# Kernel optimization log

Hardware: AMD Instinct MI355X
Metric: run time of the kernel (lower is better)

Reference implementation:

```python
import jax, jax.numpy as jnp
import numpy as np

N_NODES = 50000
N_EDGES = 800000
NUM_GRAPHS = 64
NEG_SLOPE = 0.2


def gatv2_layer(x, src, dst, Wl, bl, Wr, br, att, b_out, heads, out_ch, concat):
    # PyG GATv2Conv: x_j = lin_l(x)[src], x_i = lin_r(x)[dst]
    N = x.shape[0]
    xl = (x @ Wl + bl).reshape(N, heads, out_ch)
    xr = (x @ Wr + br).reshape(N, heads, out_ch)
    m = xl[src] + xr[dst]                                  # [E, H, C]
    e = jax.nn.leaky_relu(m, negative_slope=NEG_SLOPE)
    logits = jnp.einsum('ehc,hc->eh', e, att)              # [E, H]
    # softmax over incoming edges of each destination node
    seg_max = jax.ops.segment_max(logits, dst, num_segments=N)
    ex = jnp.exp(logits - seg_max[dst])
    denom = jax.ops.segment_sum(ex, dst, num_segments=N)
    alpha = ex / denom[dst]                                # [E, H]
    out = jax.ops.segment_sum(alpha[..., None] * xl[src], dst, num_segments=N)
    out = out.reshape(N, heads * out_ch) if concat else out.mean(axis=1)
    return out + b_out


def _forward(x, edge_index, batch,
             Wl1, bl1, Wr1, br1, att1, b1,
             Wl2, bl2, Wr2, br2, att2, b2,
             Wl3, bl3, Wr3, br3, att3, b3,
             Wm1, bm1, Wm2, bm2):
    N = x.shape[0]
    loops = jnp.arange(N, dtype=edge_index.dtype)
    src = jnp.concatenate([edge_index[0], loops])          # add_self_loops=True
    dst = jnp.concatenate([edge_index[1], loops])
    h = jax.nn.relu(gatv2_layer(x, src, dst, Wl1, bl1, Wr1, br1, att1, b1, 4, 64, True))
    h = jax.nn.relu(gatv2_layer(h, src, dst, Wl2, bl2, Wr2, br2, att2, b2, 2, 64, True))
    h = jax.nn.relu(gatv2_layer(h, src, dst, Wl3, bl3, Wr3, br3, att3, b3, 1, 64, False))
    # global_mean_pool
    sums = jax.ops.segment_sum(h, batch, num_segments=NUM_GRAPHS)
    counts = jax.ops.segment_sum(jnp.ones((N, 1), h.dtype), batch, num_segments=NUM_GRAPHS)
    pooled = sums / jnp.maximum(counts, 1.0)
    return jax.nn.relu(pooled @ Wm1 + bm1) @ Wm2 + bm2


def setup_inputs() -> dict:
    key = jax.random.key(0)
    ks = jax.random.split(key, 24)
    s = 0.05
    inp = {
        'x': jax.random.normal(ks[0], (N_NODES, 128), jnp.float32),
        'edge_index': jax.random.randint(ks[1], (2, N_EDGES), 0, N_NODES, jnp.int64),
        'batch': jnp.sort(jax.random.randint(ks[2], (N_NODES,), 0, NUM_GRAPHS, jnp.int64)),
        # conv1: in=128, heads=4, C=64
        'Wl1': jax.random.normal(ks[3], (128, 256), jnp.float32) * s,
        'bl1': jnp.zeros((256,), jnp.float32),
        'Wr1': jax.random.normal(ks[4], (128, 256), jnp.float32) * s,
        'br1': jnp.zeros((256,), jnp.float32),
        'att1': jax.random.normal(ks[5], (4, 64), jnp.float32) * s,
        'b1': jnp.zeros((256,), jnp.float32),
        # conv2: in=256, heads=2, C=64
        'Wl2': jax.random.normal(ks[6], (256, 128), jnp.float32) * s,
        'bl2': jnp.zeros((128,), jnp.float32),
        'Wr2': jax.random.normal(ks[7], (256, 128), jnp.float32) * s,
        'br2': jnp.zeros((128,), jnp.float32),
        'att2': jax.random.normal(ks[8], (2, 64), jnp.float32) * s,
        'b2': jnp.zeros((128,), jnp.float32),
        # conv3: in=128, heads=1, C=64, concat=False
        'Wl3': jax.random.normal(ks[9], (128, 64), jnp.float32) * s,
        'bl3': jnp.zeros((64,), jnp.float32),
        'Wr3': jax.random.normal(ks[10], (128, 64), jnp.float32) * s,
        'br3': jnp.zeros((64,), jnp.float32),
        'att3': jax.random.normal(ks[11], (1, 64), jnp.float32) * s,
        'b3': jnp.zeros((64,), jnp.float32),
        # MLP 64 -> 32 -> 2
        'Wm1': jax.random.normal(ks[12], (64, 32), jnp.float32) * s,
        'bm1': jnp.zeros((32,), jnp.float32),
        'Wm2': jax.random.normal(ks[13], (32, 2), jnp.float32) * s,
        'bm2': jnp.zeros((2,), jnp.float32),
    }
    return inp


def reference(x, edge_index, batch,
              Wl1, bl1, Wr1, br1, att1, b1,
              Wl2, bl2, Wr2, br2, att2, b2,
              Wl3, bl3, Wr3, br3, att3, b3,
              Wm1, bm1, Wm2, bm2):
    return _forward(x, edge_index, batch,
                    Wl1, bl1, Wr1, br1, att1, b1,
                    Wl2, bl2, Wr2, br2, att2, b2,
                    Wl3, bl3, Wr3, br3, att3, b3,
                    Wm1, bm1, Wm2, bm2)
```

## Files before the change

### kernel.cpp

```cpp
#include <hip/hip_runtime.h>


typedef __attribute__((ext_vector_type(8))) short bf16x8;
typedef __attribute__((ext_vector_type(4))) float f32x4;

#define SORT_BLOCKS 64
#define SCAN_BLOCKS 256

__device__ inline unsigned short f2bf(float f) {
    unsigned u = __float_as_uint(f);
    unsigned r = (u + 0x7fff + ((u >> 16) & 1)) >> 16;
    return (unsigned short)r;
}

__device__ inline void unpack8(uint4 a, float* d) {
    d[0] = __uint_as_float(a.x << 16); d[1] = __uint_as_float(a.x & 0xffff0000u);
    d[2] = __uint_as_float(a.y << 16); d[3] = __uint_as_float(a.y & 0xffff0000u);
    d[4] = __uint_as_float(a.z << 16); d[5] = __uint_as_float(a.z & 0xffff0000u);
    d[6] = __uint_as_float(a.w << 16); d[7] = __uint_as_float(a.w & 0xffff0000u);
}

__global__ void cvt_kernel(const float* __restrict__ in,
                           unsigned short* __restrict__ out, int n)
{
    int i = (blockIdx.x * blockDim.x + threadIdx.x) * 4;
    if (i >= n) return;
    float4 v = *reinterpret_cast<const float4*>(in + i);
    ushort4 o;
    o.x = f2bf(v.x); o.y = f2bf(v.y); o.z = f2bf(v.z); o.w = f2bf(v.w);
    *reinterpret_cast<ushort4*>(out + i) = o;
}

__global__ void cvt_wt_all_kernel(
    const float* __restrict__ Wl1, const float* __restrict__ Wr1, unsigned short* __restrict__ T1l, unsigned short* __restrict__ T1r,
    const float* __restrict__ Wl2, const float* __restrict__ Wr2, unsigned short* __restrict__ T2l, unsigned short* __restrict__ T2r,
    const float* __restrict__ Wl3, const float* __restrict__ Wr3, unsigned short* __restrict__ T3l, unsigned short* __restrict__ T3r)
{
    int id = blockIdx.x * blockDim.x + threadIdx.x;
    const float* W; unsigned short* T; int K, No, idx;
    if (id < 2 * 32768) {
        K = 128; No = 256; idx = id & 32767;
        W = (id < 32768) ? Wl1 : Wr1; T = (id < 32768) ? T1l : T1r;
    } else if (id < 2 * 32768 + 2 * 32768) {
        int v = id - 65536; K = 256; No = 128; idx = v & 32767;
        W = (v < 32768) ? Wl2 : Wr2; T = (v < 32768) ? T2l : T2r;
    } else {
        int v = id - 131072; if (v >= 2 * 8192) return;
        K = 128; No = 64; idx = v & 8191;
        W = (v < 8192) ? Wl3 : Wr3; T = (v < 8192) ? T3l : T3r;
    }
    int n = idx / K, k = idx - n * K;
    T[idx] = f2bf(W[(size_t)k * No + n]);
}

template <int K, int NY>
__global__ __launch_bounds__(256) void gemm_slab(
    const unsigned short* __restrict__ A,
    const unsigned short* __restrict__ W0, const unsigned short* __restrict__ W1,
    const float* __restrict__ bias0, const float* __restrict__ bias1,
    unsigned short* __restrict__ OutL, unsigned short* __restrict__ OutR,
    int M)
{
    constexpr int CPR = K / 8;
    __shared__ __align__(16) char As[64 * K * 2];
    __shared__ __align__(16) char Bs[64 * 128 * 2];

    const int t = threadIdx.x;
    const int lane = t & 63;
    const int wid = t >> 6;
    const int row0 = blockIdx.x * 64;

    #pragma unroll
    for (int i = 0; i < (64 * CPR) / 256; ++i) {
        int c16 = i * 256 + t;
        int r = c16 / CPR, j = c16 % CPR;
        int gr = row0 + r; if (gr > M - 1) gr = M - 1;
        uint4 v = *reinterpret_cast<const uint4*>(A + (size_t)gr * K + j * 8);
        *reinterpret_cast<uint4*>(As + r * (2 * K) + ((j ^ (r & 7)) << 4)) = v;
    }

    const int ra = wid * 16 + (lane & 15);
    const int rowA_byte = ra * (2 * K);

    for (int z = 0; z < 2; ++z) {
        const unsigned short* Wt = z ? W1 : W0;
        const float* bias = z ? bias1 : bias0;
        unsigned short* Out = z ? OutR : OutL;
        for (int y = 0; y < NY; ++y) {
            f32x4 acc[4];
            #pragma unroll
            for (int j = 0; j < 4; ++j) acc[j] = (f32x4){0.f, 0.f, 0.f, 0.f};

            #pragma unroll
            for (int kh = 0; kh < K / 128; ++kh) {
                __syncthreads();
                #pragma unroll
                for (int i = 0; i < 4; ++i) {
                    int c16 = i * 256 + t;
                    int n = c16 >> 4, j = c16 & 15;
                    uint4 v = *reinterpret_cast<const uint4*>(
                        Wt + (size_t)(y * 64 + n) * K + kh * 128 + j * 8);
                    *reinterpret_cast<uint4*>(Bs + n * 256 + ((j ^ (n & 7)) << 4)) = v;
                }
                __syncthreads();
                #pragma unroll
                for (int ks = 0; ks < 4; ++ks) {
                    int chA = kh * 16 + ks * 4 + (lane >> 4);
                    bf16x8 a = *reinterpret_cast<const bf16x8*>(
                        As + rowA_byte + ((chA ^ (ra & 7)) << 4));
                    #pragma unroll
                    for (int j = 0; j < 4; ++j) {
                        int nb = j * 16 + (lane & 15);
                        int chB = ks * 4 + (lane >> 4);
                        bf16x8 b = *reinterpret_cast<const bf16x8*>(
                            Bs + nb * 256 + ((chB ^ (nb & 7)) << 4));
                        acc[j] = __builtin_amdgcn_mfma_f32_16x16x32_bf16(a, b, acc[j], 0, 0, 0);
                    }
                }
            }
            __syncthreads();
            #pragma unroll
            for (int j = 0; j < 4; ++j) {
                float bb = bias[y * 64 + j * 16 + (lane & 15)];
                #pragma unroll
                for (int q = 0; q < 4; ++q) {
                    int r = wid * 16 + (lane >> 4) * 4 + q;
                    int c = j * 16 + (lane & 15);
                    *reinterpret_cast<unsigned short*>(Bs + r * 128 + c * 2)
                        = f2bf(acc[j][q] + bb);
                }
            }
            __syncthreads();
            {
                int r = t >> 2, ch = t & 3;
                int gr = row0 + r;
                if (gr < M) {
                    const uint4* src = reinterpret_cast<const uint4*>(Bs + r * 128 + ch * 32);
                    uint4 v0 = src[0], v1 = src[1];
                    uint4* dst = reinterpret_cast<uint4*>(
                        Out + ((size_t)y * M + gr) * 64 + ch * 16);
                    dst[0] = v0; dst[1] = v1;
                }
            }
        }
    }
}

__global__ void hist_kernel(const int* __restrict__ ei, int E, int Etot,
                            int* __restrict__ deg)
{
    int i = blockIdx.x * blockDim.x + threadIdx.x;
    if (i >= Etot) return;
    int d = (i < E) ? ei[E + i] : (i - E);
    atomicAdd(&deg[d], 1);
}

__global__ __launch_bounds__(256) void scan1_kernel(
    const int* __restrict__ deg, int* __restrict__ blockSums, int N)
{
    __shared__ int red[256];
    const int b = blockIdx.x, t = threadIdx.x;
    const int chunk = (N + SCAN_BLOCKS - 1) / SCAN_BLOCKS;
    const int lo = b * chunk;
    const int hi = (lo + chunk < N) ? lo + chunk : N;
    int s = 0;
    for (int i = lo + t; i < hi; i += 256) s += deg[i];
    red[t] = s;
    __syncthreads();
    #pragma unroll
    for (int off = 128; off > 0; off >>= 1) {
        if (t < off) red[t] += red[t + off];
        __syncthreads();
    }
    if (t == 0) blockSums[b] = red[0];
}

__global__ __launch_bounds__(256) void scan2_kernel(
    const int* __restrict__ blockSums, int* __restrict__ blockBase,
    int* __restrict__ rowptr, int N)
{
    __shared__ int tmp[256];
    const int t = threadIdx.x;
    int v = blockSums[t];
    tmp[t] = v;
    __syncthreads();
    for (int off = 1; off < 256; off <<= 1) {
        int u = (t >= off) ? tmp[t - off] : 0;
        __syncthreads();
        tmp[t] += u;
        __syncthreads();
    }
    blockBase[t] = tmp[t] - v;
    if (t == 255) rowptr[N] = tmp[255];
}

__global__ __launch_bounds__(256) void scan3_kernel(
    const int* __restrict__ deg, const int* __restrict__ blockBase,
    int* __restrict__ rowptr, int* __restrict__ cursor, int N)
{
    __shared__ int tmp[256];
    __shared__ int carry;
    const int b = blockIdx.x, t = threadIdx.x;
    const int chunk = (N + SCAN_BLOCKS - 1) / SCAN_BLOCKS;
    const int lo = b * chunk;
    const int hi = (lo + chunk < N) ? lo + chunk : N;
    if (t == 0) carry = blockBase[b];
    __syncthreads();
    for (int j = lo; j < hi; j += 256) {
        int i = j + t;
        int v = (i < hi) ? deg[i] : 0;
        tmp[t] = v;
        __syncthreads();
        for (int off = 1; off < 256; off <<= 1) {
            int u = (t >= off) ? tmp[t - off] : 0;
            __syncthreads();
            tmp[t] += u;
            __syncthreads();
        }
        int excl = carry + tmp[t] - v;
        if (i < hi) { rowptr[i] = excl; cursor[i] = excl; }
        __syncthreads();
        if (t == 255) carry += tmp[255];
        __syncthreads();
    }
}

__global__ void scatter_kernel(const int* __restrict__ ei, int E, int Etot,
                               int* __restrict__ cursor, int* __restrict__ ssrc)
{
    int i = blockIdx.x * blockDim.x + threadIdx.x;
    if (i >= Etot) return;
    int d, s;
    if (i < E) { s = ei[i]; d = ei[E + i]; }
    else       { s = i - E; d = s; }
    int pos = atomicAdd(&cursor[d], 1);
    ssrc[pos] = s;
}

__global__ __launch_bounds__(256) void dhist2_kernel(
    const int* __restrict__ rowptr, int* __restrict__ blockHist, int N)
{
    __shared__ int lh[256];
    lh[threadIdx.x] = 0;
    __syncthreads();
    const int chunk = (N + SORT_BLOCKS - 1) / SORT_BLOCKS;
    const int lo = blockIdx.x * chunk;
    const int hi = (lo + chunk < N) ? lo + chunk : N;
    for (int d = lo + threadIdx.x; d < hi; d += 256) {
        int deg = rowptr[d + 1] - rowptr[d];
        atomicAdd(&lh[deg > 255 ? 255 : deg], 1);
    }
    __syncthreads();
    blockHist[blockIdx.x * 256 + threadIdx.x] = lh[threadIdx.x];
}

__global__ __launch_bounds__(256) void dscan2_kernel(
    const int* __restrict__ blockHist, int* __restrict__ blockOff)
{
    const int t = threadIdx.x;
    int total = 0;
    for (int b = 0; b < SORT_BLOCKS; ++b) total += blockHist[b * 256 + t];
    __shared__ int tmp[256];
    tmp[t] = total;
    __syncthreads();
    for (int off = 1; off < 256; off <<= 1) {
        int v = (t >= off) ? tmp[t - off] : 0;
        __syncthreads();
        tmp[t] += v;
        __syncthreads();
    }
    int grand = tmp[255];
    int start = grand - tmp[t];
    for (int b = 0; b < SORT_BLOCKS; ++b) {
        blockOff[b * 256 + t] = start;
        start += blockHist[b * 256 + t];
    }
}

__global__ __launch_bounds__(256) void dscatter2_kernel(
    const int* __restrict__ rowptr, const int* __restrict__ blockOff,
    int* __restrict__ dperm, int N)
{
    __shared__ int cur[256];
    cur[threadIdx.x] = blockOff[blockIdx.x * 256 + threadIdx.x];
    __syncthreads();
    const int chunk = (N + SORT_BLOCKS - 1) / SORT_BLOCKS;
    const int lo = blockIdx.x * chunk;
    const int hi = (lo + chunk < N) ? lo + chunk : N;
    for (int d = lo + threadIdx.x; d < hi; d += 256) {
        int deg = rowptr[d + 1] - rowptr[d];
        int pos = atomicAdd(&cur[deg > 255 ? 255 : deg], 1);
        dperm[pos] = d;
    }
}

template <int H, bool OUT_F32, bool OUT_BF16>
__global__ __launch_bounds__(256) void gat_fused4(
    const int* __restrict__ rowptr, const int* __restrict__ ssrc,
    const int* __restrict__ dperm,
    const unsigned short* __restrict__ xl, const unsigned short* __restrict__ xr,
    const float* __restrict__ att, const float* __restrict__ bias,
    float* __restrict__ outf, unsigned short* __restrict__ outb, int N)
{
    const int gid = blockIdx.x * 64 + (threadIdx.x >> 2);
    const int sub = threadIdx.x & 3;
    if (gid >= N * H) return;
    const int h  = gid / N;
    const int di = gid - h * N;
    const int d  = dperm[di];
    const int HC = H * 64;
    const int so = sub * 16;

    const unsigned short* xlh = xl + (size_t)h * N * 64;

    float xrv[16], attv[16], acc[16];
    {
        const unsigned short* pr = xr + ((size_t)h * N + d) * 64 + so;
        uint4 v0 = *reinterpret_cast<const uint4*>(pr);
        uint4 v1 = *reinterpret_cast<const uint4*>(pr + 8);
        unpack8(v0, xrv); unpack8(v1, xrv + 8);
        const float* pa = att + h * 64 + so;
        #pragma unroll
        for (int k = 0; k < 16; k += 4) {
            float4 w = *reinterpret_cast<const float4*>(pa + k);
            attv[k] = w.x; attv[k+1] = w.y; attv[k+2] = w.z; attv[k+3] = w.w;
        }
    }
    #pragma unroll
    for (int k = 0; k < 16; ++k) acc[k] = 0.f;
    float M = -3.0e38f, S = 0.f;

    const int begin = rowptr[d], end = rowptr[d + 1];
    uint4 c0, c1;
    {
        const unsigned short* pl = xlh + (size_t)ssrc[begin] * 64 + so;
        c0 = *reinterpret_cast<const uint4*>(pl);
        c1 = *reinterpret_cast<const uint4*>(pl + 8);
    }
    for (int e = begin; e < end; ++e) {
        uint4 n0, n1;
        const bool more = (e + 1 < end);
        if (more) {
            const unsigned short* pl = xlh + (size_t)ssrc[e + 1] * 64 + so;
            n0 = *reinterpret_cast<const uint4*>(pl);
            n1 = *reinterpret_cast<const uint4*>(pl + 8);
        }
        float cur[16];
        unpack8(c0, cur);
        unpack8(c1, cur + 8);
        float p = 0.f;
        #pragma unroll
        for (int k = 0; k < 16; ++k) {
            float v = cur[k] + xrv[k];
            v = fmaxf(v, 0.2f * v);
            p = fmaf(v, attv[k], p);
        }
        p += __shfl_xor(p, 1);
        p += __shfl_xor(p, 2);
        float nM = fmaxf(M, p);
        float scale = __expf(M - nM);
        float w = __expf(p - nM);
        S = fmaf(S, scale, w);
        #pragma unroll
        for (int k = 0; k < 16; ++k) acc[k] = fmaf(acc[k], scale, w * cur[k]);
        M = nM;
        if (more) { c0 = n0; c1 = n1; }
    }
    float inv = 1.f / S;
    const float* pb = bias + h * 64 + so;
    #pragma unroll
    for (int k = 0; k < 16; ++k) {
        float val = fmaf(acc[k], inv, pb[k]);
        acc[k] = val > 0.f ? val : 0.f;
    }
    size_t ob = (size_t)d * HC + h * 64 + so;
    if (OUT_F32) {
        #pragma unroll
        for (int k = 0; k < 16; k += 4) {
            float4 v = {acc[k], acc[k+1], acc[k+2], acc[k+3]};
            *reinterpret_cast<float4*>(outf + ob + k) = v;
        }
    }
    if (OUT_BF16) {
        unsigned pk[8];
        #pragma unroll
        for (int k = 0; k < 8; ++k)
            pk[k] = (unsigned)f2bf(acc[2*k]) | ((unsigned)f2bf(acc[2*k+1]) << 16);
        uint4 lo = {pk[0], pk[1], pk[2], pk[3]};
        uint4 hi = {pk[4], pk[5], pk[6], pk[7]};
        *reinterpret_cast<uint4*>(outb + ob) = lo;
        *reinterpret_cast<uint4*>(outb + ob + 8) = hi;
    }
}

__global__ __launch_bounds__(256) void pool_kernel2(
    const float* __restrict__ h3, const int* __restrict__ batch,
    float* __restrict__ sums, float* __restrict__ counts, int N)
{
    const int wave = blockIdx.x * 4 + (threadIdx.x >> 6);
    const int lane = threadIdx.x & 63;
    const int n0 = wave * 64;
    if (n0 >= N) return;
    const int n1 = (n0 + 64 < N) ? n0 + 64 : N;
    float s = 0.f, cnt = 0.f;
    int g = batch[n0];
    for (int n = n0; n < n1; ++n) {
        int gn = batch[n];
        if (gn != g) {
            atomicAdd(&sums[g * 64 + lane], s);
            if (lane == 0) atomicAdd(&counts[g], cnt);
            s = 0.f; cnt = 0.f; g = gn;
        }
        s += h3[(size_t)n * 64 + lane];
        cnt += 1.f;
    }
    atomicAdd(&sums[g * 64 + lane], s);
    if (lane == 0) atomicAdd(&counts[g], cnt);
}

__global__ __launch_bounds__(64) void mlp_kernel(
    const float* __restrict__ sums, const float* __restrict__ counts,
    const float* __restrict__ Wm1, const float* __restrict__ bm1,
    const float* __restrict__ Wm2, const float* __restrict__ bm2,
    float* __restrict__ out)
{
    int g = blockIdx.x;
    int t = threadIdx.x;
    __shared__ float pooled[64];
    __shared__ float hidden[32];
    float cnt = counts[g];
    cnt = cnt > 1.f ? cnt : 1.f;
    pooled[t] = sums[g * 64 + t] / cnt;
    __syncthreads();
    if (t < 32) {
        float a = bm1[t];
        #pragma unroll
        for (int k = 0; k < 64; ++k) a = fmaf(pooled[k], Wm1[k * 32 + t], a);
        hidden[t] = a > 0.f ? a : 0.f;
    }
    __syncthreads();
    if (t < 2) {
        float a = bm2[t];
        #pragma unroll
        for (int j = 0; j < 32; ++j) a = fmaf(hidden[j], Wm2[j * 2 + t], a);
        out[g * 2 + t] = a;
    }
}

static void run_layer(const unsigned short* Xb, int K, int H,
                      const float* bl, const float* br,
                      const float* att, const float* bias_out,
                      const unsigned short* Wtl, const unsigned short* Wtr,
                      const int* rowptr, const int* ssrc, const int* dperm, int N,
                      unsigned short* xl, unsigned short* xr,
                      float* houtf, unsigned short* houtb,
                      hipStream_t stream)
{
    int gblocks = (N + 63) / 64;
    if (K == 128 && H == 4)
        gemm_slab<128, 4><<<gblocks, 256, 0, stream>>>(Xb, Wtl, Wtr, bl, br, xl, xr, N);
    else if (K == 256)
        gemm_slab<256, 2><<<gblocks, 256, 0, stream>>>(Xb, Wtl, Wtr, bl, br, xl, xr, N);
    else
        gemm_slab<128, 1><<<gblocks, 256, 0, stream>>>(Xb, Wtl, Wtr, bl, br, xl, xr, N);

    int ngroups = N * H;
    int blocks = (ngroups + 63) / 64;
    if (H == 4)
        gat_fused4<4, false, true><<<blocks, 256, 0, stream>>>(
            rowptr, ssrc, dperm, xl, xr, att, bias_out, houtf, houtb, N);
    else if (H == 2)
        gat_fused4<2, false, true><<<blocks, 256, 0, stream>>>(
            rowptr, ssrc, dperm, xl, xr, att, bias_out, houtf, houtb, N);
    else
        gat_fused4<1, true, false><<<blocks, 256, 0, stream>>>(
            rowptr, ssrc, dperm, xl, xr, att, bias_out, houtf, houtb, N);
}

extern "C" void kernel_launch(void* const* d_in, const int* in_sizes, int n_in,
                              void* d_out, int out_size, void* d_ws, size_t ws_size,
                              hipStream_t stream)
{
    const float* x    = (const float*)d_in[0];
    const int*   ei   = (const int*)d_in[1];
    const int*   batch= (const int*)d_in[2];
    const float* Wl1 = (const float*)d_in[3];
    const float* bl1 = (const float*)d_in[4];
    const float* Wr1 = (const float*)d_in[5];
    const float* br1 = (const float*)d_in[6];
    const float* att1= (const float*)d_in[7];
    const float* b1  = (const float*)d_in[8];
    const float* Wl2 = (const float*)d_in[9];
    const float* bl2 = (const float*)d_in[10];
    const float* Wr2 = (const float*)d_in[11];
    const float* br2 = (const float*)d_in[12];
    const float* att2= (const float*)d_in[13];
    const float* b2  = (const float*)d_in[14];
    const float* Wl3 = (const float*)d_in[15];
    const float* bl3 = (const float*)d_in[16];
    const float* Wr3 = (const float*)d_in[17];
    const float* br3 = (const float*)d_in[18];
    const float* att3= (const float*)d_in[19];
    const float* b3  = (const float*)d_in[20];
    const float* Wm1 = (const float*)d_in[21];
    const float* bm1 = (const float*)d_in[22];
    const float* Wm2 = (const float*)d_in[23];
    const float* bm2 = (const float*)d_in[24];

    const int N    = in_sizes[2];
    const int E    = in_sizes[1] / 2;
    const int Etot = E + N;
    const int K1   = in_sizes[0] / N;

    char* wsb = (char*)d_ws;
    size_t o = 0;
    auto alloc = [&](size_t bytes) { char* p = wsb + o; o += (bytes + 255) & ~(size_t)255; return p; };
    unsigned short* xl    = (unsigned short*)alloc((size_t)N * 256 * 2);
    unsigned short* xr    = (unsigned short*)alloc((size_t)N * 256 * 2);
    unsigned short* xb    = (unsigned short*)alloc((size_t)N * K1 * 2);
    unsigned short* h1b   = (unsigned short*)alloc((size_t)N * 256 * 2);
    unsigned short* h2b   = (unsigned short*)alloc((size_t)N * 128 * 2);
    float*          h3f   = (float*)alloc((size_t)N * 64 * 4);
    int*   deg    = (int*)alloc((size_t)N * 4);
    int*   rowptr = (int*)alloc((size_t)(N + 1) * 4);
    int*   cursor = (int*)alloc((size_t)N * 4);
    int*   ssrc   = (int*)alloc((size_t)Etot * 4);
    int*   dperm  = (int*)alloc((size_t)N * 4);
    int*   blockHist = (int*)alloc((size_t)SORT_BLOCKS * 256 * 4);
    int*   blockOff  = (int*)alloc((size_t)SORT_BLOCKS * 256 * 4);
    int*   blockSums = (int*)alloc((size_t)SCAN_BLOCKS * 4);
    int*   blockBase = (int*)alloc((size_t)SCAN_BLOCKS * 4);
    unsigned short* Wt1l = (unsigned short*)alloc(128 * 256 * 2);
    unsigned short* Wt1r = (unsigned short*)alloc(128 * 256 * 2);
    unsigned short* Wt2l = (unsigned short*)alloc(256 * 128 * 2);
    unsigned short* Wt2r = (unsigned short*)alloc(256 * 128 * 2);
    unsigned short* Wt3l = (unsigned short*)alloc(128 * 64 * 2);
    unsigned short* Wt3r = (unsigned short*)alloc(128 * 64 * 2);
    float* sums   = (float*)alloc(64 * 64 * 4);
    float* counts = (float*)alloc(64 * 4);
    (void)ws_size; (void)n_in; (void)out_size;

    hipMemsetAsync(deg, 0, (size_t)N * 4, stream);
    hist_kernel<<<(Etot + 255) / 256, 256, 0, stream>>>(ei, E, Etot, deg);
    scan1_kernel<<<SCAN_BLOCKS, 256, 0, stream>>>(deg, blockSums, N);
    scan2_kernel<<<1, 256, 0, stream>>>(blockSums, blockBase, rowptr, N);
    scan3_kernel<<<SCAN_BLOCKS, 256, 0, stream>>>(deg, blockBase, rowptr, cursor, N);
    scatter_kernel<<<(Etot + 255) / 256, 256, 0, stream>>>(ei, E, Etot, cursor, ssrc);
    dhist2_kernel<<<SORT_BLOCKS, 256, 0, stream>>>(rowptr, blockHist, N);
    dscan2_kernel<<<1, 256, 0, stream>>>(blockHist, blockOff);
    dscatter2_kernel<<<SORT_BLOCKS, 256, 0, stream>>>(rowptr, blockOff, dperm, N);

    cvt_kernel<<<((N * K1) / 4 + 255) / 256, 256, 0, stream>>>(x, xb, N * K1);
    cvt_wt_all_kernel<<<(147456 + 255) / 256, 256, 0, stream>>>(
        Wl1, Wr1, Wt1l, Wt1r, Wl2, Wr2, Wt2l, Wt2r, Wl3, Wr3, Wt3l, Wt3r);

    run_layer(xb, K1, 4, bl1, br1, att1, b1, Wt1l, Wt1r,
              rowptr, ssrc, dperm, N, xl, xr, nullptr, h1b, stream);
    run_layer(h1b, 256, 2, bl2, br2, att2, b2, Wt2l, Wt2r,
              rowptr, ssrc, dperm, N, xl, xr, nullptr, h2b, stream);
    run_layer(h2b, 128, 1, bl3, br3, att3, b3, Wt3l, Wt3r,
              rowptr, ssrc, dperm, N, xl, xr, h3f, nullptr, stream);

    hipMemsetAsync(sums, 0, 64 * 64 * 4, stream);
    hipMemsetAsync(counts, 0, 64 * 4, stream);
    {
        int waves = (N + 63) / 64;
        pool_kernel2<<<(waves + 3) / 4, 256, 0, stream>>>(h3f, batch, sums, counts, N);
    }
    mlp_kernel<<<64, 64, 0, stream>>>(sums, counts, Wm1, bm1, Wm2, bm2, (float*)d_out);
}
```

Before: 357.2 us.

## Switch intermediates from bf16 to fp16 and use packed half math in edge loop

Changes all intermediate activations and weights from bf16 to fp16, uses the fp16 MFMA in the projection GEMM, and rewrites the per-edge attention loop to use packed half2 add/max/mul and fdot2 instead of unpacking to fp32. The aim is to halve the ALU work per edge in the gather-bound attention kernel while keeping the same memory traffic. The risk is lower range: the softmax accumulator is kept in fp16, which can lose precision or overflow with large activations.

```diff
diff --git a/kernel.cpp b/kernel.cpp
--- a/kernel.cpp
+++ b/kernel.cpp
@@ -1,43 +1,37 @@
 #include <hip/hip_runtime.h>
 
 
-typedef __attribute__((ext_vector_type(8))) short bf16x8;
-typedef __attribute__((ext_vector_type(4))) float f32x4;
+typedef _Float16 half_t;
+typedef _Float16 h2    __attribute__((ext_vector_type(2)));
+typedef _Float16 f16x8 __attribute__((ext_vector_type(8)));
+typedef float    f32x4 __attribute__((ext_vector_type(4)));
 
 #define SORT_BLOCKS 64
 #define SCAN_BLOCKS 256
 
-__device__ inline unsigned short f2bf(float f) {
-    unsigned u = __float_as_uint(f);
-    unsigned r = (u + 0x7fff + ((u >> 16) & 1)) >> 16;
-    return (unsigned short)r;
-}
-
-__device__ inline void unpack8(uint4 a, float* d) {
-    d[0] = __uint_as_float(a.x << 16); d[1] = __uint_as_float(a.x & 0xffff0000u);
-    d[2] = __uint_as_float(a.y << 16); d[3] = __uint_as_float(a.y & 0xffff0000u);
-    d[4] = __uint_as_float(a.z << 16); d[5] = __uint_as_float(a.z & 0xffff0000u);
-    d[6] = __uint_as_float(a.w << 16); d[7] = __uint_as_float(a.w & 0xffff0000u);
-}
+#if __has_builtin(__builtin_amdgcn_fdot2)
+#define FDOT2(a, b, c) __builtin_amdgcn_fdot2((a), (b), (c), false)
+#else
+#define FDOT2(a, b, c) ((c) + (float)(a)[0] * (float)(b)[0] + (float)(a)[1] * (float)(b)[1])
+#endif
 
 __global__ void cvt_kernel(const float* __restrict__ in,
-                           unsigned short* __restrict__ out, int n)
+                           half_t* __restrict__ out, int n)
 {
     int i = (blockIdx.x * blockDim.x + threadIdx.x) * 4;
     if (i >= n) return;
     float4 v = *reinterpret_cast<const float4*>(in + i);
-    ushort4 o;
-    o.x = f2bf(v.x); o.y = f2bf(v.y); o.z = f2bf(v.z); o.w = f2bf(v.w);
-    *reinterpret_cast<ushort4*>(out + i) = o;
+    half_t o[4] = {(half_t)v.x, (half_t)v.y, (half_t)v.z, (half_t)v.w};
+    *reinterpret_cast<uint2*>(out + i) = *reinterpret_cast<const uint2*>(o);
 }
 
 __global__ void cvt_wt_all_kernel(
-    const float* __restrict__ Wl1, const float* __restrict__ Wr1, unsigned short* __restrict__ T1l, unsigned short* __restrict__ T1r,
-    const float* __restrict__ Wl2, const float* __restrict__ Wr2, unsigned short* __restrict__ T2l, unsigned short* __restrict__ T2r,
-    const float* __restrict__ Wl3, const float* __restrict__ Wr3, unsigned short* __restrict__ T3l, unsigned short* __restrict__ T3r)
+    const float* __restrict__ Wl1, const float* __restrict__ Wr1, half_t* __restrict__ T1l, half_t* __restrict__ T1r,
+    const float* __restrict__ Wl2, const float* __restrict__ Wr2, half_t* __restrict__ T2l, half_t* __restrict__ T2r,
+    const float* __restrict__ Wl3, const float* __restrict__ Wr3, half_t* __restrict__ T3l, half_t* __restrict__ T3r)
 {
     int id = blockIdx.x * blockDim.x + threadIdx.x;
-    const float* W; unsigned short* T; int K, No, idx;
+    const float* W; half_t* T; int K, No, idx;
     if (id < 2 * 32768) {
         K = 128; No = 256; idx = id & 32767;
         W = (id < 32768) ? Wl1 : Wr1; T = (id < 32768) ? T1l : T1r;
@@ -50,15 +44,15 @@
         W = (v < 8192) ? Wl3 : Wr3; T = (v < 8192) ? T3l : T3r;
     }
     int n = idx / K, k = idx - n * K;
-    T[idx] = f2bf(W[(size_t)k * No + n]);
+    T[idx] = (half_t)W[(size_t)k * No + n];
 }
 
 template <int K, int NY>
 __global__ __launch_bounds__(256) void gemm_slab(
-    const unsigned short* __restrict__ A,
-    const unsigned short* __restrict__ W0, const unsigned short* __restrict__ W1,
+    const half_t* __restrict__ A,
+    const half_t* __restrict__ W0, const half_t* __restrict__ W1,
     const float* __restrict__ bias0, const float* __restrict__ bias1,
-    unsigned short* __restrict__ OutL, unsigned short* __restrict__ OutR,
+    half_t* __restrict__ OutL, half_t* __restrict__ OutR,
     int M)
 {
     constexpr int CPR = K / 8;
@@ -83,9 +77,9 @@
     const int rowA_byte = ra * (2 * K);
 
     for (int z = 0; z < 2; ++z) {
-        const unsigned short* Wt = z ? W1 : W0;
+        const half_t* Wt = z ? W1 : W0;
         const float* bias = z ? bias1 : bias0;
-        unsigned short* Out = z ? OutR : OutL;
+        half_t* Out = z ? OutR : OutL;
         for (int y = 0; y < NY; ++y) {
             f32x4 acc[4];
             #pragma unroll
@@ -106,15 +100,15 @@
                 #pragma unroll
                 for (int ks = 0; ks < 4; ++ks) {
                     int chA = kh * 16 + ks * 4 + (lane >> 4);
-                    bf16x8 a = *reinterpret_cast<const bf16x8*>(
+                    f16x8 a = *reinterpret_cast<const f16x8*>(
                         As + rowA_byte + ((chA ^ (ra & 7)) << 4));
                     #pragma unroll
                     for (int j = 0; j < 4; ++j) {
                         int nb = j * 16 + (lane & 15);
                         int chB = ks * 4 + (lane >> 4);
-                        bf16x8 b = *reinterpret_cast<const bf16x8*>(
+                        f16x8 b = *reinterpret_cast<const f16x8*>(
                             Bs + nb * 256 + ((chB ^ (nb & 7)) << 4));
-                        acc[j] = __builtin_amdgcn_mfma_f32_16x16x32_bf16(a, b, acc[j], 0, 0, 0);
+                        acc[j] = __builtin_amdgcn_mfma_f32_16x16x32_f16(a, b, acc[j], 0, 0, 0);
                     }
                 }
             }
@@ -126,8 +120,8 @@
                 for (int q = 0; q < 4; ++q) {
                     int r = wid * 16 + (lane >> 4) * 4 + q;
                     int c = j * 16 + (lane & 15);
-                    *reinterpret_cast<unsigned short*>(Bs + r * 128 + c * 2)
-                        = f2bf(acc[j][q] + bb);
+                    *reinterpret_cast<half_t*>(Bs + r * 128 + c * 2)
+                        = (half_t)(acc[j][q] + bb);
                 }
             }
             __syncthreads();
@@ -294,13 +288,13 @@
     }
 }
 
-template <int H, bool OUT_F32, bool OUT_BF16>
+template <int H, bool OUT_F32, bool OUT_F16>
 __global__ __launch_bounds__(256) void gat_fused4(
     const int* __restrict__ rowptr, const int* __restrict__ ssrc,
     const int* __restrict__ dperm,
-    const unsigned short* __restrict__ xl, const unsigned short* __restrict__ xr,
+    const half_t* __restrict__ xl, const half_t* __restrict__ xr,
     const float* __restrict__ att, const float* __restrict__ bias,
-    float* __restrict__ outf, unsigned short* __restrict__ outb, int N)
+    float* __restrict__ outf, half_t* __restrict__ outb, int N)
 {
     const int gid = blockIdx.x * 64 + (threadIdx.x >> 2);
     const int sub = threadIdx.x & 3;
@@ -311,49 +305,48 @@
     const int HC = H * 64;
     const int so = sub * 16;
 
-    const unsigned short* xlh = xl + (size_t)h * N * 64;
-
-    float xrv[16], attv[16], acc[16];
+    const half_t* xlh = xl + (size_t)h * N * 64;
+    const h2 c02 = {(half_t)0.2f, (half_t)0.2f};
+
+    h2 xrv[8], attv[8], acc[8];
     {
-        const unsigned short* pr = xr + ((size_t)h * N + d) * 64 + so;
-        uint4 v0 = *reinterpret_cast<const uint4*>(pr);
-        uint4 v1 = *reinterpret_cast<const uint4*>(pr + 8);
-        unpack8(v0, xrv); unpack8(v1, xrv + 8);
+        const half_t* pr = xr + ((size_t)h * N + d) * 64 + so;
+        uint4 rb[2];
+        rb[0] = *reinterpret_cast<const uint4*>(pr);
+        rb[1] = *reinterpret_cast<const uint4*>(pr + 8);
+        const h2* rp = reinterpret_cast<const h2*>(rb);
         const float* pa = att + h * 64 + so;
         #pragma unroll
-        for (int k = 0; k < 16; k += 4) {
-            float4 w = *reinterpret_cast<const float4*>(pa + k);
-            attv[k] = w.x; attv[k+1] = w.y; attv[k+2] = w.z; attv[k+3] = w.w;
-        }
-    }
-    #pragma unroll
-    for (int k = 0; k < 16; ++k) acc[k] = 0.f;
+        for (int k = 0; k < 8; ++k) {
+            xrv[k] = rp[k];
+            attv[k] = (h2){(half_t)pa[2 * k], (half_t)pa[2 * k + 1]};
+            acc[k] = (h2){(half_t)0.f, (half_t)0.f};
+        }
+    }
     float M = -3.0e38f, S = 0.f;
 
     const int begin = rowptr[d], end = rowptr[d + 1];
-    uint4 c0, c1;
+    uint4 cbuf[2];
     {
-        const unsigned short* pl = xlh + (size_t)ssrc[begin] * 64 + so;
-        c0 = *reinterpret_cast<const uint4*>(pl);
-        c1 = *reinterpret_cast<const uint4*>(pl + 8);
+        const half_t* pl = xlh + (size_t)ssrc[begin] * 64 + so;
+        cbuf[0] = *reinterpret_cast<const uint4*>(pl);
+        cbuf[1] = *reinterpret_cast<const uint4*>(pl + 8);
     }
     for (int e = begin; e < end; ++e) {
-        uint4 n0, n1;
+        uint4 nbuf[2];
         const bool more = (e + 1 < end);
         if (more) {
-            const unsigned short* pl = xlh + (size_t)ssrc[e + 1] * 64 + so;
-            n0 = *reinterpret_cast<const uint4*>(pl);
-            n1 = *reinterpret_cast<const uint4*>(pl + 8);
-        }
-        float cur[16];
-        unpack8(c0, cur);
-        unpack8(c1, cur + 8);
+            const half_t* pl = xlh + (size_t)ssrc[e + 1] * 64 + so;
+            nbuf[0] = *reinterpret_cast<const uint4*>(pl);
+            nbuf[1] = *reinterpret_cast<const uint4*>(pl + 8);
+        }
+        const h2* cur = reinterpret_cast<const h2*>(cbuf);
         float p = 0.f;
         #pragma unroll
-        for (int k = 0; k < 16; ++k) {
-            float v = cur[k] + xrv[k];
-            v = fmaxf(v, 0.2f * v);
-            p = fmaf(v, attv[k], p);
+        for (int k = 0; k < 8; ++k) {
+            h2 m = cur[k] + xrv[k];
+            h2 v = __builtin_elementwise_max(m, m * c02);
+            p = FDOT2(v, attv[k], p);
         }
         p += __shfl_xor(p, 1);
         p += __shfl_xor(p, 2);
@@ -361,35 +354,38 @@
         float scale = __expf(M - nM);
         float w = __expf(p - nM);
         S = fmaf(S, scale, w);
-        #pragma unroll
-        for (int k = 0; k < 16; ++k) acc[k] = fmaf(acc[k], scale, w * cur[k]);
+        h2 s2 = {(half_t)scale, (half_t)scale};
+        h2 w2 = {(half_t)w, (half_t)w};
+        #pragma unroll
+        for (int k = 0; k < 8; ++k) acc[k] = acc[k] * s2 + cur[k] * w2;
         M = nM;
-        if (more) { c0 = n0; c1 = n1; }
+        if (more) { cbuf[0] = nbuf[0]; cbuf[1] = nbuf[1]; }
     }
     float inv = 1.f / S;
     const float* pb = bias + h * 64 + so;
+    float res[16];
     #pragma unroll
-    for (int k = 0; k < 16; ++k) {
-        float val = fmaf(acc[k], inv, pb[k]);
-        acc[k] = val > 0.f ? val : 0.f;
+    for (int k = 0; k < 8; ++k) {
+        float v0 = fmaf((float)acc[k][0], inv, pb[2 * k]);
+        float v1 = fmaf((float)acc[k][1], inv, pb[2 * k + 1]);
+        res[2 * k]     = v0 > 0.f ? v0 : 0.f;
+        res[2 * k + 1] = v1 > 0.f ? v1 : 0.f;
     }
     size_t ob = (size_t)d * HC + h * 64 + so;
     if (OUT_F32) {
         #pragma unroll
         for (int k = 0; k < 16; k += 4) {
-            float4 v = {acc[k], acc[k+1], acc[k+2], acc[k+3]};
+            float4 v = {res[k], res[k+1], res[k+2], res[k+3]};
             *reinterpret_cast<float4*>(outf + ob + k) = v;
         }
     }
-    if (OUT_BF16) {
-        unsigned pk[8];
-        #pragma unroll
-        for (int k = 0; k < 8; ++k)
-            pk[k] = (unsigned)f2bf(acc[2*k]) | ((unsigned)f2bf(acc[2*k+1]) << 16);
-        uint4 lo = {pk[0], pk[1], pk[2], pk[3]};
-        uint4 hi = {pk[4], pk[5], pk[6], pk[7]};
-        *reinterpret_cast<uint4*>(outb + ob) = lo;
-        *reinterpret_cast<uint4*>(outb + ob + 8) = hi;
+    if (OUT_F16) {
+        half_t o[16];
+        #pragma unroll
+        for (int k = 0; k < 16; ++k) o[k] = (half_t)res[k];
+        const uint4* ov = reinterpret_cast<const uint4*>(o);
+        *reinterpret_cast<uint4*>(outb + ob) = ov[0];
+        *reinterpret_cast<uint4*>(outb + ob + 8) = ov[1];
     }
 }
 
@@ -447,13 +443,13 @@
     }
 }
 
-static void run_layer(const unsigned short* Xb, int K, int H,
+static void run_layer(const half_t* Xb, int K, int H,
                       const float* bl, const float* br,
                       const float* att, const float* bias_out,
-                      const unsigned short* Wtl, const unsigned short* Wtr,
+                      const half_t* Wtl, const half_t* Wtr,
                       const int* rowptr, const int* ssrc, const int* dperm, int N,
-                      unsigned short* xl, unsigned short* xr,
-                      float* houtf, unsigned short* houtb,
+                      half_t* xl, half_t* xr,
+                      float* houtf, half_t* houtb,
                       hipStream_t stream)
 {
     int gblocks = (N + 63) / 64;
@@ -515,12 +511,12 @@
     char* wsb = (char*)d_ws;
     size_t o = 0;
     auto alloc = [&](size_t bytes) { char* p = wsb + o; o += (bytes + 255) & ~(size_t)255; return p; };
-    unsigned short* xl    = (unsigned short*)alloc((size_t)N * 256 * 2);
-    unsigned short* xr    = (unsigned short*)alloc((size_t)N * 256 * 2);
-    unsigned short* xb    = (unsigned short*)alloc((size_t)N * K1 * 2);
-    unsigned short* h1b   = (unsigned short*)alloc((size_t)N * 256 * 2);
-    unsigned short* h2b   = (unsigned short*)alloc((size_t)N * 128 * 2);
-    float*          h3f   = (float*)alloc((size_t)N * 64 * 4);
+    half_t* xl    = (half_t*)alloc((size_t)N * 256 * 2);
+    half_t* xr    = (half_t*)alloc((size_t)N * 256 * 2);
+    half_t* xb    = (half_t*)alloc((size_t)N * K1 * 2);
+    half_t* h1b   = (half_t*)alloc((size_t)N * 256 * 2);
+    half_t* h2b   = (half_t*)alloc((size_t)N * 128 * 2);
+    float*  h3f   = (float*)alloc((size_t)N * 64 * 4);
     int*   deg    = (int*)alloc((size_t)N * 4);
     int*   rowptr = (int*)alloc((size_t)(N + 1) * 4);
     int*   cursor = (int*)alloc((size_t)N * 4);
@@ -530,12 +526,12 @@
     int*   blockOff  = (int*)alloc((size_t)SORT_BLOCKS * 256 * 4);
     int*   blockSums = (int*)alloc((size_t)SCAN_BLOCKS * 4);
     int*   blockBase = (int*)alloc((size_t)SCAN_BLOCKS * 4);
-    unsigned short* Wt1l = (unsigned short*)alloc(128 * 256 * 2);
-    unsigned short* Wt1r = (unsigned short*)alloc(128 * 256 * 2);
-    unsigned short* Wt2l = (unsigned short*)alloc(256 * 128 * 2);
-    unsigned short* Wt2r = (unsigned short*)alloc(256 * 128 * 2);
-    unsigned short* Wt3l = (unsigned short*)alloc(128 * 64 * 2);
-    unsigned short* Wt3r = (unsigned short*)alloc(128 * 64 * 2);
+    half_t* Wt1l = (half_t*)alloc(128 * 256 * 2);
+    half_t* Wt1r = (half_t*)alloc(128 * 256 * 2);
+    half_t* Wt2l = (half_t*)alloc(256 * 128 * 2);
+    half_t* Wt2r = (half_t*)alloc(256 * 128 * 2);
+    half_t* Wt3l = (half_t*)alloc(128 * 64 * 2);
+    half_t* Wt3r = (half_t*)alloc(128 * 64 * 2);
     float* sums   = (float*)alloc(64 * 64 * 4);
     float* counts = (float*)alloc(64 * 4);
     (void)ws_size; (void)n_in; (void)out_size;
```

Measured after the change: 375.8 us. +5.2%, slower.

## Fuse preprocessing, scan, and pool+MLP kernels to cut launch count

Applied to the files above, without the earlier changes.

Folds the memsets, input conversion and weight transposition into one grid-stride prep kernel. It removes the single-block scan2 and dscan2 kernels by having each block recompute the prefix over the block sums. Pooling and the MLP are merged using a last-block-done atomic counter. The aim is to remove about seven small launches and memsets from the serialized stream, at the cost of redundant per-block scan work and a grid-wide completion pattern.

```diff
diff --git a/kernel.cpp b/kernel.cpp
--- a/kernel.cpp
+++ b/kernel.cpp
@@ -20,37 +20,50 @@
     d[6] = __uint_as_float(a.w << 16); d[7] = __uint_as_float(a.w & 0xffff0000u);
 }
 
-__global__ void cvt_kernel(const float* __restrict__ in,
-                           unsigned short* __restrict__ out, int n)
-{
-    int i = (blockIdx.x * blockDim.x + threadIdx.x) * 4;
-    if (i >= n) return;
-    float4 v = *reinterpret_cast<const float4*>(in + i);
-    ushort4 o;
-    o.x = f2bf(v.x); o.y = f2bf(v.y); o.z = f2bf(v.z); o.w = f2bf(v.w);
-    *reinterpret_cast<ushort4*>(out + i) = o;
-}
-
-__global__ void cvt_wt_all_kernel(
-    const float* __restrict__ Wl1, const float* __restrict__ Wr1, unsigned short* __restrict__ T1l, unsigned short* __restrict__ T1r,
-    const float* __restrict__ Wl2, const float* __restrict__ Wr2, unsigned short* __restrict__ T2l, unsigned short* __restrict__ T2r,
-    const float* __restrict__ Wl3, const float* __restrict__ Wr3, unsigned short* __restrict__ T3l, unsigned short* __restrict__ T3r)
-{
-    int id = blockIdx.x * blockDim.x + threadIdx.x;
-    const float* W; unsigned short* T; int K, No, idx;
-    if (id < 2 * 32768) {
-        K = 128; No = 256; idx = id & 32767;
-        W = (id < 32768) ? Wl1 : Wr1; T = (id < 32768) ? T1l : T1r;
-    } else if (id < 2 * 32768 + 2 * 32768) {
-        int v = id - 65536; K = 256; No = 128; idx = v & 32767;
-        W = (v < 32768) ? Wl2 : Wr2; T = (v < 32768) ? T2l : T2r;
-    } else {
-        int v = id - 131072; if (v >= 2 * 8192) return;
-        K = 128; No = 64; idx = v & 8191;
-        W = (v < 8192) ? Wl3 : Wr3; T = (v < 8192) ? T3l : T3r;
-    }
-    int n = idx / K, k = idx - n * K;
-    T[idx] = f2bf(W[(size_t)k * No + n]);
+__global__ __launch_bounds__(256) void prep_kernel(
+    const float* __restrict__ x, int N, int K1,
+    unsigned short* __restrict__ xb,
+    const float* __restrict__ Wl1, const float* __restrict__ Wr1,
+    unsigned short* __restrict__ T1l, unsigned short* __restrict__ T1r,
+    const float* __restrict__ Wl2, const float* __restrict__ Wr2,
+    unsigned short* __restrict__ T2l, unsigned short* __restrict__ T2r,
+    const float* __restrict__ Wl3, const float* __restrict__ Wr3,
+    unsigned short* __restrict__ T3l, unsigned short* __restrict__ T3r,
+    int* __restrict__ deg, float* __restrict__ sums,
+    float* __restrict__ counts, int* __restrict__ done)
+{
+    const int gtid = blockIdx.x * 256 + threadIdx.x;
+    const int gsz = (int)gridDim.x * 256;
+
+    for (int i = gtid; i < N; i += gsz) deg[i] = 0;
+    if (gtid < 64 * 64) sums[gtid] = 0.f;
+    if (gtid < 64) counts[gtid] = 0.f;
+    if (gtid == 0) *done = 0;
+
+    {
+        int n4 = (N * K1) >> 2;
+        for (int i = gtid; i < n4; i += gsz) {
+            float4 v = *reinterpret_cast<const float4*>(x + (size_t)i * 4);
+            ushort4 o;
+            o.x = f2bf(v.x); o.y = f2bf(v.y); o.z = f2bf(v.z); o.w = f2bf(v.w);
+            *reinterpret_cast<ushort4*>(xb + (size_t)i * 4) = o;
+        }
+    }
+    for (int id = gtid; id < 147456; id += gsz) {
+        const float* W; unsigned short* T; int K, No, idx;
+        if (id < 65536) {
+            K = 128; No = 256; idx = id & 32767;
+            W = (id < 32768) ? Wl1 : Wr1; T = (id < 32768) ? T1l : T1r;
+        } else if (id < 131072) {
+            int v = id - 65536; K = 256; No = 128; idx = v & 32767;
+            W = (v < 32768) ? Wl2 : Wr2; T = (v < 32768) ? T2l : T2r;
+        } else {
+            int v = id - 131072; K = 128; No = 64; idx = v & 8191;
+            W = (v < 8192) ? Wl3 : Wr3; T = (v < 8192) ? T3l : T3r;
+        }
+        int n = idx / K, k = idx - n * K;
+        T[idx] = f2bf(W[(size_t)k * No + n]);
+    }
 }
 
 template <int K, int NY>
@@ -175,52 +188,42 @@
     if (t == 0) blockSums[b] = red[0];
 }
 
-__global__ __launch_bounds__(256) void scan2_kernel(
-    const int* __restrict__ blockSums, int* __restrict__ blockBase,
-    int* __restrict__ rowptr, int N)
-{
-    __shared__ int tmp[256];
-    const int t = threadIdx.x;
-    int v = blockSums[t];
-    tmp[t] = v;
-    __syncthreads();
-    for (int off = 1; off < 256; off <<= 1) {
-        int u = (t >= off) ? tmp[t - off] : 0;
-        __syncthreads();
-        tmp[t] += u;
-        __syncthreads();
-    }
-    blockBase[t] = tmp[t] - v;
-    if (t == 255) rowptr[N] = tmp[255];
-}
-
-__global__ __launch_bounds__(256) void scan3_kernel(
-    const int* __restrict__ deg, const int* __restrict__ blockBase,
+__global__ __launch_bounds__(256) void scan3b_kernel(
+    const int* __restrict__ deg, const int* __restrict__ blockSums,
     int* __restrict__ rowptr, int* __restrict__ cursor, int N)
 {
-    __shared__ int tmp[256];
-    __shared__ int carry;
+    __shared__ int sh[256];
     const int b = blockIdx.x, t = threadIdx.x;
     const int chunk = (N + SCAN_BLOCKS - 1) / SCAN_BLOCKS;
     const int lo = b * chunk;
     const int hi = (lo + chunk < N) ? lo + chunk : N;
-    if (t == 0) carry = blockBase[b];
-    __syncthreads();
+
+    sh[t] = blockSums[t];
+    __syncthreads();
+    for (int off = 1; off < 256; off <<= 1) {
+        int u = (t >= off) ? sh[t - off] : 0;
+        __syncthreads();
+        sh[t] += u;
+        __syncthreads();
+    }
+    if (b == 0 && t == 255) rowptr[N] = sh[255];
+    int carry = (b == 0) ? 0 : sh[b - 1];
+    __syncthreads();
+
     for (int j = lo; j < hi; j += 256) {
         int i = j + t;
         int v = (i < hi) ? deg[i] : 0;
-        tmp[t] = v;
+        sh[t] = v;
         __syncthreads();
         for (int off = 1; off < 256; off <<= 1) {
-            int u = (t >= off) ? tmp[t - off] : 0;
+            int u = (t >= off) ? sh[t - off] : 0;
             __syncthreads();
-            tmp[t] += u;
+            sh[t] += u;
             __syncthreads();
         }
-        int excl = carry + tmp[t] - v;
+        int excl = carry + sh[t] - v;
         if (i < hi) { rowptr[i] = excl; cursor[i] = excl; }
-        __syncthreads();
-        if (t == 255) carry += tmp[255];
+        carry += sh[255];
         __syncthreads();
     }
 }
@@ -254,40 +257,36 @@
     blockHist[blockIdx.x * 256 + threadIdx.x] = lh[threadIdx.x];
 }
 
-__global__ __launch_bounds__(256) void dscan2_kernel(
-    const int* __restrict__ blockHist, int* __restrict__ blockOff)
-{
-    const int t = threadIdx.x;
-    int total = 0;
-    for (int b = 0; b < SORT_BLOCKS; ++b) total += blockHist[b * 256 + t];
-    __shared__ int tmp[256];
-    tmp[t] = total;
+__global__ __launch_bounds__(256) void dscatter2b_kernel(
+    const int* __restrict__ rowptr, const int* __restrict__ blockHist,
+    int* __restrict__ dperm, int N)
+{
+    __shared__ int sh[256];
+    __shared__ int cur[256];
+    const int b = blockIdx.x, t = threadIdx.x;
+
+    int total = 0, myoff = 0;
+    for (int bb = 0; bb < SORT_BLOCKS; ++bb) {
+        int hv = blockHist[bb * 256 + t];
+        if (bb < b) myoff += hv;
+        total += hv;
+    }
+    sh[t] = total;
     __syncthreads();
     for (int off = 1; off < 256; off <<= 1) {
-        int v = (t >= off) ? tmp[t - off] : 0;
-        __syncthreads();
-        tmp[t] += v;
-        __syncthreads();
-    }
-    int grand = tmp[255];
-    int start = grand - tmp[t];
-    for (int b = 0; b < SORT_BLOCKS; ++b) {
-        blockOff[b * 256 + t] = start;
-        start += blockHist[b * 256 + t];
-    }
-}
-
-__global__ __launch_bounds__(256) void dscatter2_kernel(
-    const int* __restrict__ rowptr, const int* __restrict__ blockOff,
-    int* __restrict__ dperm, int N)
-{
-    __shared__ int cur[256];
-    cur[threadIdx.x] = blockOff[blockIdx.x * 256 + threadIdx.x];
-    __syncthreads();
+        int u = (t >= off) ? sh[t - off] : 0;
+        __syncthreads();
+        sh[t] += u;
+        __syncthreads();
+    }
+    int grand = sh[255];
+    cur[t] = (grand - sh[t]) + myoff;
+    __syncthreads();
+
     const int chunk = (N + SORT_BLOCKS - 1) / SORT_BLOCKS;
-    const int lo = blockIdx.x * chunk;
+    const int lo = b * chunk;
     const int hi = (lo + chunk < N) ? lo + chunk : N;
-    for (int d = lo + threadIdx.x; d < hi; d += 256) {
+    for (int d = lo + t; d < hi; d += 256) {
         int deg = rowptr[d + 1] - rowptr[d];
         int pos = atomicAdd(&cur[deg > 255 ? 255 : deg], 1);
         dperm[pos] = d;
@@ -393,57 +392,64 @@
     }
 }
 
-__global__ __launch_bounds__(256) void pool_kernel2(
+__global__ __launch_bounds__(256) void pool_mlp_kernel(
     const float* __restrict__ h3, const int* __restrict__ batch,
-    float* __restrict__ sums, float* __restrict__ counts, int N)
-{
-    const int wave = blockIdx.x * 4 + (threadIdx.x >> 6);
-    const int lane = threadIdx.x & 63;
-    const int n0 = wave * 64;
-    if (n0 >= N) return;
-    const int n1 = (n0 + 64 < N) ? n0 + 64 : N;
-    float s = 0.f, cnt = 0.f;
-    int g = batch[n0];
-    for (int n = n0; n < n1; ++n) {
-        int gn = batch[n];
-        if (gn != g) {
-            atomicAdd(&sums[g * 64 + lane], s);
-            if (lane == 0) atomicAdd(&counts[g], cnt);
-            s = 0.f; cnt = 0.f; g = gn;
-        }
-        s += h3[(size_t)n * 64 + lane];
-        cnt += 1.f;
-    }
-    atomicAdd(&sums[g * 64 + lane], s);
-    if (lane == 0) atomicAdd(&counts[g], cnt);
-}
-
-__global__ __launch_bounds__(64) void mlp_kernel(
-    const float* __restrict__ sums, const float* __restrict__ counts,
+    float* __restrict__ sums, float* __restrict__ counts,
+    int* __restrict__ done, int nblocks,
     const float* __restrict__ Wm1, const float* __restrict__ bm1,
     const float* __restrict__ Wm2, const float* __restrict__ bm2,
-    float* __restrict__ out)
-{
-    int g = blockIdx.x;
-    int t = threadIdx.x;
-    __shared__ float pooled[64];
-    __shared__ float hidden[32];
-    float cnt = counts[g];
-    cnt = cnt > 1.f ? cnt : 1.f;
-    pooled[t] = sums[g * 64 + t] / cnt;
-    __syncthreads();
-    if (t < 32) {
-        float a = bm1[t];
-        #pragma unroll
-        for (int k = 0; k < 64; ++k) a = fmaf(pooled[k], Wm1[k * 32 + t], a);
-        hidden[t] = a > 0.f ? a : 0.f;
-    }
-    __syncthreads();
-    if (t < 2) {
-        float a = bm2[t];
-        #pragma unroll
-        for (int j = 0; j < 32; ++j) a = fmaf(hidden[j], Wm2[j * 2 + t], a);
-        out[g * 2 + t] = a;
+    float* __restrict__ out, int N)
+{
+    const int wid = threadIdx.x >> 6;
+    const int lane = threadIdx.x & 63;
+    const int wave = blockIdx.x * 4 + wid;
+    const int n0 = wave * 64;
+    if (n0 < N) {
+        const int n1 = (n0 + 64 < N) ? n0 + 64 : N;
+        float s = 0.f, cnt = 0.f;
+        int g = batch[n0];
+        for (int n = n0; n < n1; ++n) {
+            int gn = batch[n];
+            if (gn != g) {
+                atomicAdd(&sums[g * 64 + lane], s);
+                if (lane == 0) atomicAdd(&counts[g], cnt);
+                s = 0.f; cnt = 0.f; g = gn;
+            }
+            s += h3[(size_t)n * 64 + lane];
+            cnt += 1.f;
+        }
+        atomicAdd(&sums[g * 64 + lane], s);
+        if (lane == 0) atomicAdd(&counts[g], cnt);
+    }
+    __threadfence();
+    __syncthreads();
+    __shared__ int lastFlag;
+    if (threadIdx.x == 0)
+        lastFlag = (atomicAdd(done, 1) == nblocks - 1);
+    __syncthreads();
+    if (!lastFlag) return;
+    __threadfence();
+
+    __shared__ float pl[4][64];
+    __shared__ float hd[4][32];
+    for (int g = wid; g < 64; g += 4) {
+        float cnt = fmaxf(counts[g], 1.f);
+        pl[wid][lane] = sums[g * 64 + lane] / cnt;
+        __syncthreads();
+        if (lane < 32) {
+            float a = bm1[lane];
+            #pragma unroll
+            for (int k = 0; k < 64; ++k) a = fmaf(pl[wid][k], Wm1[k * 32 + lane], a);
+            hd[wid][lane] = fmaxf(a, 0.f);
+        }
+        __syncthreads();
+        if (lane < 2) {
+            float a = bm2[lane];
+            #pragma unroll
+            for (int j = 0; j < 32; ++j) a = fmaf(hd[wid][j], Wm2[j * 2 + lane], a);
+            out[g * 2 + lane] = a;
+        }
+        __syncthreads();
     }
 }
 
@@ -527,9 +533,7 @@
     int*   ssrc   = (int*)alloc((size_t)Etot * 4);
     int*   dperm  = (int*)alloc((size_t)N * 4);
     int*   blockHist = (int*)alloc((size_t)SORT_BLOCKS * 256 * 4);
-    int*   blockOff  = (int*)alloc((size_t)SORT_BLOCKS * 256 * 4);
     int*   blockSums = (int*)alloc((size_t)SCAN_BLOCKS * 4);
-    int*   blockBase = (int*)alloc((size_t)SCAN_BLOCKS * 4);
     unsigned short* Wt1l = (unsigned short*)alloc(128 * 256 * 2);
     unsigned short* Wt1r = (unsigned short*)alloc(128 * 256 * 2);
     unsigned short* Wt2l = (unsigned short*)alloc(256 * 128 * 2);
@@ -538,21 +542,20 @@
     unsigned short* Wt3r = (unsigned short*)alloc(128 * 64 * 2);
     float* sums   = (float*)alloc(64 * 64 * 4);
     float* counts = (float*)alloc(64 * 4);
+    int*   done   = (int*)alloc(256);
     (void)ws_size; (void)n_in; (void)out_size;
 
-    hipMemsetAsync(deg, 0, (size_t)N * 4, stream);
+    prep_kernel<<<1024, 256, 0, stream>>>(
+        x, N, K1, xb,
+        Wl1, Wr1, Wt1l, Wt1r, Wl2, Wr2, Wt2l, Wt2r, Wl3, Wr3, Wt3l, Wt3r,
+        deg, sums, counts, done);
+
     hist_kernel<<<(Etot + 255) / 256, 256, 0, stream>>>(ei, E, Etot, deg);
     scan1_kernel<<<SCAN_BLOCKS, 256, 0, stream>>>(deg, blockSums, N);
-    scan2_kernel<<<1, 256, 0, stream>>>(blockSums, blockBase, rowptr, N);
-    scan3_kernel<<<SCAN_BLOCKS, 256, 0, stream>>>(deg, blockBase, rowptr, cursor, N);
+    scan3b_kernel<<<SCAN_BLOCKS, 256, 0, stream>>>(deg, blockSums, rowptr, cursor, N);
     scatter_kernel<<<(Etot + 255) / 256, 256, 0, stream>>>(ei, E, Etot, cursor, ssrc);
     dhist2_kernel<<<SORT_BLOCKS, 256, 0, stream>>>(rowptr, blockHist, N);
-    dscan2_kernel<<<1, 256, 0, stream>>>(blockHist, blockOff);
-    dscatter2_kernel<<<SORT_BLOCKS, 256, 0, stream>>>(rowptr, blockOff, dperm, N);
-
-    cvt_kernel<<<((N * K1) / 4 + 255) / 256, 256, 0, stream>>>(x, xb, N * K1);
-    cvt_wt_all_kernel<<<(147456 + 255) / 256, 256, 0, stream>>>(
-        Wl1, Wr1, Wt1l, Wt1r, Wl2, Wr2, Wt2l, Wt2r, Wl3, Wr3, Wt3l, Wt3r);
+    dscatter2b_kernel<<<SORT_BLOCKS, 256, 0, stream>>>(rowptr, blockHist, dperm, N);
 
     run_layer(xb, K1, 4, bl1, br1, att1, b1, Wt1l, Wt1r,
               rowptr, ssrc, dperm, N, xl, xr, nullptr, h1b, stream);
@@ -561,11 +564,11 @@
     run_layer(h2b, 128, 1, bl3, br3, att3, b3, Wt3l, Wt3r,
               rowptr, ssrc, dperm, N, xl, xr, h3f, nullptr, stream);
 
-    hipMemsetAsync(sums, 0, 64 * 64 * 4, stream);
-    hipMemsetAsync(counts, 0, 64 * 4, stream);
     {
         int waves = (N + 63) / 64;
-        pool_kernel2<<<(waves + 3) / 4, 256, 0, stream>>>(h3f, batch, sums, counts, N);
-    }
-    mlp_kernel<<<64, 64, 0, stream>>>(sums, counts, Wm1, bm1, Wm2, bm2, (float*)d_out);
-}
+        int nblocks = (waves + 3) / 4;
+        pool_mlp_kernel<<<nblocks, 256, 0, stream>>>(
+            h3f, batch, sums, counts, done, nblocks, Wm1, bm1, Wm2, bm2,
+            (float*)d_out, N);
+    }
+}
```

After: 396.2 us. +10.9%, slower.
